# Performance work log

Measured on AMD Instinct MI355X. Metric: run time of the kernel, lower is better.

Reference implementation:

```python
import jax, jax.numpy as jnp
import numpy as np

B, L, DIM, H = 2, 2048, 2048, 16
D = DIM // H  # head_dim = 128
EPS = 1e-6


def _rope_freqs(seq_len: int, head_dim: int, theta: float = 10000.0) -> jnp.ndarray:
    # Flux-style rotation matrix: [1, 1, L, D/2, 2, 2]
    pos = np.arange(seq_len, dtype=np.float32)
    inv = 1.0 / (theta ** (np.arange(0, head_dim, 2, dtype=np.float32) / head_dim))
    ang = np.einsum('l,d->ld', pos, inv)  # [L, D/2]
    cos, sin = np.cos(ang), np.sin(ang)
    rot = np.stack([np.stack([cos, -sin], -1), np.stack([sin, cos], -1)], -2)  # [L, D/2, 2, 2]
    return jnp.asarray(rot[None, None])


def _rms_norm(x, scale):
    rrms = jax.lax.rsqrt(jnp.mean(jnp.square(x), axis=-1, keepdims=True) + EPS)
    return x * rrms * scale


def _apply_rope(xq, xk, freqs_cis):
    # xq/xk: [B, H, L, D]; freqs_cis: [1, 1, L, D/2, 2, 2]
    def rot(x):
        xr = x.reshape(*x.shape[:-1], -1, 1, 2)  # [B,H,L,D/2,1,2]
        out = freqs_cis[..., 0] * xr[..., 0] + freqs_cis[..., 1] * xr[..., 1]
        return out.reshape(x.shape)
    return rot(xq), rot(xk)


def setup_inputs() -> dict:
    key = jax.random.key(0)
    ks = jax.random.split(key, 4)
    x = jax.random.normal(ks[0], (B, L, DIM), dtype=jnp.float32)
    qkv_w = jax.random.normal(ks[1], (DIM, 3 * DIM), dtype=jnp.float32) * 0.02
    qkv_b = jnp.zeros((3 * DIM,), dtype=jnp.float32)
    q_scale = jnp.ones((D,), dtype=jnp.float32)
    k_scale = jnp.ones((D,), dtype=jnp.float32)
    proj_w = jax.random.normal(ks[2], (DIM, DIM), dtype=jnp.float32) * 0.02
    proj_b = jnp.zeros((DIM,), dtype=jnp.float32)
    pe = _rope_freqs(L, D)
    return {"x": x, "pe": pe, "qkv_w": qkv_w, "qkv_b": qkv_b,
            "q_scale": q_scale, "k_scale": k_scale,
            "proj_w": proj_w, "proj_b": proj_b}


def reference(x, pe, qkv_w, qkv_b, q_scale, k_scale, proj_w, proj_b):
    b, l, _ = x.shape
    qkv = x @ qkv_w + qkv_b                      # [B, L, 3*DIM]
    qkv = qkv.reshape(b, l, 3, H, D)
    qkv = jnp.transpose(qkv, (2, 0, 3, 1, 4))    # [3, B, H, L, D]
    q, k, v = qkv[0], qkv[1], qkv[2]
    q = _rms_norm(q, q_scale)
    k = _rms_norm(k, k_scale)
    q, k = _apply_rope(q, k, pe)
    scores = jnp.einsum('bhqd,bhkd->bhqk', q, k) / jnp.sqrt(jnp.float32(D))
    attn = jax.nn.softmax(scores, axis=-1)
    o = jnp.einsum('bhqk,bhkd->bhqd', attn, v)   # [B, H, L, D]
    o = jnp.transpose(o, (0, 2, 1, 3)).reshape(b, l, H * D)
    return o @ proj_w + proj_b
```

## Files before the change

kernel.cpp:

```cpp
#include <hip/hip_runtime.h>
#include <cstdint>
#include <cstddef>

#define BB 2
#define HB 16
#define LL 2048
#define DD 128
#define MM 4096
#define KK 2048
#define N1 6144
#define N2 2048
#define BHLD (BB*HB*LL*DD)

typedef unsigned short u16;
typedef __bf16 bf16x8 __attribute__((ext_vector_type(8)));
typedef short  s16x4  __attribute__((ext_vector_type(4)));
typedef float  f32x4  __attribute__((ext_vector_type(4)));

typedef __attribute__((address_space(1))) void* as1_ptr;
typedef __attribute__((address_space(3))) void* as3_ptr;

__device__ __forceinline__ void gload16(const void* g, void* l) {
  __builtin_amdgcn_global_load_lds((as1_ptr)g, (as3_ptr)l, 16, 0, 0);
}

__device__ __forceinline__ float bf2f(u16 u) {
  union { unsigned v; float f; } c; c.v = ((unsigned)u) << 16; return c.f;
}
__device__ __forceinline__ u16 f2bf(float f) {
  unsigned u = __builtin_bit_cast(unsigned, f);
  return (u16)((u + 0x7FFFu + ((u >> 16) & 1u)) >> 16);
}


__global__ __launch_bounds__(256) void f32_to_bf16_vec(
    const float* __restrict__ in, u16* __restrict__ out, int n4) {
  int i = blockIdx.x * 256 + threadIdx.x;
  if (i >= n4) return;
  float4 v = ((const float4*)in)[i];
  ushort4 o;
  o.x = f2bf(v.x); o.y = f2bf(v.y); o.z = f2bf(v.z); o.w = f2bf(v.w);
  ((ushort4*)out)[i] = o;
}

__global__ __launch_bounds__(256) void transpose_f32_bf16(
    const float* __restrict__ in, u16* __restrict__ out, int R, int C) {
  __shared__ float t[32][33];
  int c0 = blockIdx.x * 32, r0 = blockIdx.y * 32;
  int tx = threadIdx.x & 31, ty = threadIdx.x >> 5;
#pragma unroll
  for (int i = ty; i < 32; i += 8)
    t[i][tx] = in[(size_t)(r0 + i) * C + c0 + tx];
  __syncthreads();
#pragma unroll
  for (int i = ty; i < 32; i += 8)
    out[(size_t)(c0 + i) * R + r0 + tx] = f2bf(t[tx][i]);
}

template<int MODE>
__global__ __launch_bounds__(256) void gemm_bt(
    const u16* __restrict__ A, const u16* __restrict__ Bt,
    const float* __restrict__ bias, void* __restrict__ Cout,
    int Msz, int Nsz, int Ksz)
{
  __shared__ __align__(16) u16 As[128*64];
  __shared__ __align__(16) u16 Bs[128*64];
  const int tid  = threadIdx.x;
  const int lane = tid & 63;
  const int wid  = tid >> 6;
  const int l15  = lane & 15, quad = lane >> 4;
  const int m0 = blockIdx.y * 128, n0 = blockIdx.x * 128;
  const int wm = (wid >> 1) * 64, wn = (wid & 1) * 64;

  f32x4 acc[4][4] = {};

  for (int ks = 0; ks < Ksz; ks += 64) {
    __syncthreads();
#pragma unroll
    for (int j = 0; j < 4; j++) {
      const int s = (wid*4 + j)*64 + lane;
      const int row = s >> 3, pc = (s & 7) ^ (row & 7);
      gload16(&A [(size_t)(m0 + row) * Ksz + ks + pc*8], &As[(wid*4 + j)*512]);
      gload16(&Bt[(size_t)(n0 + row) * Ksz + ks + pc*8], &Bs[(wid*4 + j)*512]);
    }
    __syncthreads();
#pragma unroll
    for (int kh = 0; kh < 2; kh++) {
      bf16x8 af[4], bfr[4];
#pragma unroll
      for (int i = 0; i < 4; i++) {
        const int r = wm + i*16 + l15;
        af[i]  = *(const bf16x8*)&As[r*64 + (((kh*4 + quad) ^ (r & 7)))*8];
      }
#pragma unroll
      for (int i = 0; i < 4; i++) {
        const int r = wn + i*16 + l15;
        bfr[i] = *(const bf16x8*)&Bs[r*64 + (((kh*4 + quad) ^ (r & 7)))*8];
      }
#pragma unroll
      for (int i = 0; i < 4; i++)
#pragma unroll
        for (int j = 0; j < 4; j++)
          acc[i][j] = __builtin_amdgcn_mfma_f32_16x16x32_bf16(af[i], bfr[j], acc[i][j], 0, 0, 0);
    }
  }

#pragma unroll
  for (int i = 0; i < 4; i++) {
#pragma unroll
    for (int j = 0; j < 4; j++) {
      const int col = n0 + wn + j*16 + l15;
      const float bv = bias[col];
#pragma unroll
      for (int r = 0; r < 4; r++) {
        const int row = m0 + wm + i*16 + quad*4 + r;
        float v = acc[i][j][r] + bv;
        if (MODE == 0) {
          u16* qkv = (u16*)Cout;
          int t = col >> 11, hd = col & 2047, h = hd >> 7, d = hd & 127;
          int b = row >> 11, l = row & (LL - 1);
          size_t dst;
          if (t < 2) dst = (size_t)t * BHLD + (((size_t)(b*HB + h)) * LL + l) * DD + d;
          else       dst = (size_t)2 * BHLD + (((size_t)(b*HB + h)) * DD + d) * LL + l;
          qkv[dst] = f2bf(v);
        } else {
          ((float*)Cout)[(size_t)row * Nsz + col] = v;
        }
      }
    }
  }
}

__global__ __launch_bounds__(256) void norm_rope(
    u16* __restrict__ qkv, const float* __restrict__ pe,
    const float* __restrict__ qsc, const float* __restrict__ ksc)
{
  const int wid = threadIdx.x >> 6, lane = threadIdx.x & 63;
  const int r = blockIdx.x * 4 + wid;
  const int l = r & (LL - 1);
  const float4 p4 = *(const float4*)&pe[((size_t)l * 64 + lane) * 4];
#pragma unroll
  for (int t = 0; t < 2; t++) {
    u16* base = qkv + (size_t)t * BHLD + (size_t)r * DD + lane * 2;
    const float* sc = t ? ksc : qsc;
    ushort2 xx = *(const ushort2*)base;
    float x0 = bf2f(xx.x), x1 = bf2f(xx.y);
    float ss = x0*x0 + x1*x1;
#pragma unroll
    for (int m = 1; m < 64; m <<= 1) ss += __shfl_xor(ss, m, 64);
    float rr = rsqrtf(ss * (1.0f/128.0f) + 1e-6f);
    if (t == 0) rr *= 0.08838834764831845f;
    float y0 = x0 * rr * sc[lane*2], y1 = x1 * rr * sc[lane*2 + 1];
    ushort2 oo;
    oo.x = f2bf(p4.x * y0 + p4.y * y1);
    oo.y = f2bf(p4.z * y0 + p4.w * y1);
    *(ushort2*)base = oo;
  }
}

#define BKT 64
__global__ __launch_bounds__(256, 2) void attn(
    const u16* __restrict__ qkv, u16* __restrict__ Oout)
{
  __shared__ __align__(16) u16 Ksh[2][BKT * DD];
  __shared__ __align__(16) u16 Vsh[2][DD * BKT];

  const int bh = blockIdx.x & 31, qt = blockIdx.x >> 5;
  const int wid = threadIdx.x >> 6, lane = threadIdx.x & 63;
  const int l15 = lane & 15, quad = lane >> 4;
  const int q0 = qt * 128 + wid * 32;
  const u16* qp = qkv + (size_t)bh * LL * DD;
  const u16* kp = qkv + (size_t)BHLD + (size_t)bh * LL * DD;
  const u16* vp = qkv + (size_t)2 * BHLD + (size_t)bh * DD * LL;

  bf16x8 qb[2][4];
#pragma unroll
  for (int qf = 0; qf < 2; qf++)
#pragma unroll
    for (int f = 0; f < 4; f++)
      qb[qf][f] = *(const bf16x8*)&qp[(size_t)(q0 + qf*16 + l15) * DD + f*32 + quad*8];

  float l_acc[2] = {0.f, 0.f};
  f32x4 oacc[2][8] = {};

  auto stage = [&](int buf, int k0) {
#pragma unroll
    for (int j = 0; j < 4; j++) {
      const int s = (wid*4 + j)*64 + lane;
      {
        const int r = s >> 4, c = s & 15;
        const int lc = (c & 8) | ((c & 7) ^ (r & 7));
        gload16(&kp[(size_t)(k0 + r) * DD + lc*8], &Ksh[buf][(wid*4 + j)*512]);
      }
      {
        const int r = s >> 3, c = s & 7;
        const int lc = c ^ (r & 7);
        gload16(&vp[(size_t)r * LL + k0 + lc*8], &Vsh[buf][(wid*4 + j)*512]);
      }
    }
  };

  stage(0, 0);
  int cur = 0;

  for (int k0 = 0; k0 < LL; k0 += BKT) {
    __syncthreads();

    f32x4 s[2][4] = {};
#pragma unroll
    for (int f = 0; f < 4; f++) {
      bf16x8 kf[4];
#pragma unroll
      for (int mt = 0; mt < 4; mt++) {
        const int rr = mt*16 + l15;
        const int Lc = f*4 + quad;
        const int pc = (Lc & 8) | ((Lc & 7) ^ (rr & 7));
        kf[mt] = *(const bf16x8*)&Ksh[cur][rr*DD + pc*8];
      }
#pragma unroll
      for (int qf = 0; qf < 2; qf++)
#pragma unroll
        for (int mt = 0; mt < 4; mt++)
          s[qf][mt] = __builtin_amdgcn_mfma_f32_16x16x32_bf16(kf[mt], qb[qf][f], s[qf][mt], 0, 0, 0);
    }

    s16x4 vb[4][8];
#pragma unroll
    for (int t = 0; t < 4; t++)
#pragma unroll
      for (int c = 0; c < 8; c++) {
        const int rv = c*16 + l15;
        const int pc = (t*2 + (quad >> 1)) ^ (l15 & 7);
        vb[t][c] = *(const s16x4*)&Vsh[cur][rv*BKT + pc*8 + (quad & 1)*4];
      }

    if (k0 + BKT < LL) stage(cur ^ 1, k0 + BKT);

    s16x4 pa[2][4];
#pragma unroll
    for (int qf = 0; qf < 2; qf++) {
#pragma unroll
      for (int mt = 0; mt < 4; mt++) {
        float p0 = __expf(s[qf][mt][0] - 12.f);
        float p1 = __expf(s[qf][mt][1] - 12.f);
        float p2 = __expf(s[qf][mt][2] - 12.f);
        float p3 = __expf(s[qf][mt][3] - 12.f);
        l_acc[qf] += (p0 + p1) + (p2 + p3);
        pa[qf][mt][0] = (short)f2bf(p0); pa[qf][mt][1] = (short)f2bf(p1);
        pa[qf][mt][2] = (short)f2bf(p2); pa[qf][mt][3] = (short)f2bf(p3);
      }
    }

#pragma unroll
    for (int t = 0; t < 4; t++)
#pragma unroll
      for (int qf = 0; qf < 2; qf++)
#pragma unroll
        for (int c = 0; c < 8; c++)
          oacc[qf][c] = __builtin_amdgcn_mfma_f32_16x16x16bf16_1k(pa[qf][t], vb[t][c], oacc[qf][c], 0, 0, 0);

    cur ^= 1;
  }

#pragma unroll
  for (int qf = 0; qf < 2; qf++) {
    l_acc[qf] += __shfl_xor(l_acc[qf], 16, 64);
    l_acc[qf] += __shfl_xor(l_acc[qf], 32, 64);
  }
  const int b = bh >> 4, h = bh & 15;
#pragma unroll
  for (int qf = 0; qf < 2; qf++) {
    float lr[4];
#pragma unroll
    for (int r = 0; r < 4; r++)
      lr[r] = 1.0f / __shfl(l_acc[qf], (quad << 4) | (quad*4 + r), 64);
#pragma unroll
    for (int c = 0; c < 8; c++)
#pragma unroll
      for (int r = 0; r < 4; r++) {
        int qrow = q0 + qf*16 + quad*4 + r;
        Oout[((size_t)(b*LL + qrow)) * N2 + h*DD + c*16 + l15] = f2bf(oacc[qf][c][r] * lr[r]);
      }
  }
}


extern "C" void kernel_launch(void* const* d_in, const int* in_sizes, int n_in,
                              void* d_out, int out_size, void* d_ws, size_t ws_size,
                              hipStream_t stream) {
  const float* x       = (const float*)d_in[0];
  const float* pe      = (const float*)d_in[1];
  const float* qkv_w   = (const float*)d_in[2];
  const float* qkv_b   = (const float*)d_in[3];
  const float* q_scale = (const float*)d_in[4];
  const float* k_scale = (const float*)d_in[5];
  const float* proj_w  = (const float*)d_in[6];
  const float* proj_b  = (const float*)d_in[7];

  char* ws = (char*)d_ws;
  u16* xb   = (u16*)(ws + 0);
  u16* w1t  = (u16*)(ws + 16777216);
  u16* w2t  = (u16*)(ws + 41943040);
  u16* qkv  = (u16*)(ws + 50331648);
  u16* attO = (u16*)(ws + 100663296);

  f32_to_bf16_vec<<<(MM*KK/4)/256, 256, 0, stream>>>(x, xb, MM*KK/4);
  transpose_f32_bf16<<<dim3(N1/32, KK/32), 256, 0, stream>>>(qkv_w, w1t, KK, N1);
  transpose_f32_bf16<<<dim3(N2/32, KK/32), 256, 0, stream>>>(proj_w, w2t, KK, N2);
  gemm_bt<0><<<dim3(N1/128, MM/128), 256, 0, stream>>>(xb, w1t, qkv_b, (void*)qkv, MM, N1, KK);
  norm_rope<<<(BB*HB*LL)/4, 256, 0, stream>>>(qkv, pe, q_scale, k_scale);
  attn<<<BB*HB*(LL/128), 256, 0, stream>>>(qkv, attO);
  gemm_bt<1><<<dim3(N2/128, MM/128), 256, 0, stream>>>(attO, w2t, proj_b, d_out, MM, N2, KK);
}
```

Baseline: 442.0 us.

## Fuse RMSNorm+RoPE into QKV GEMM epilogue and merge prep kernels

Folds the per-head RMS norm and rotary embedding into the QKV GEMM epilogue. The row sum of squares is reduced across lanes and across the two N-halves of each 128-column block through shared memory, so the separate norm_rope pass that re-read and re-wrote Q and K is removed. The three conversion/transpose kernels are also merged into one launch to cut launch overhead. In exchange the epilogue gains extra shuffles, two block barriers, and per-element pe loads.

```diff
diff --git a/kernel.cpp b/kernel.cpp
--- a/kernel.cpp
+++ b/kernel.cpp
@@ -32,36 +32,42 @@
   return (u16)((u + 0x7FFFu + ((u >> 16) & 1u)) >> 16);
 }
 
-
-__global__ __launch_bounds__(256) void f32_to_bf16_vec(
-    const float* __restrict__ in, u16* __restrict__ out, int n4) {
-  int i = blockIdx.x * 256 + threadIdx.x;
-  if (i >= n4) return;
-  float4 v = ((const float4*)in)[i];
-  ushort4 o;
-  o.x = f2bf(v.x); o.y = f2bf(v.y); o.z = f2bf(v.z); o.w = f2bf(v.w);
-  ((ushort4*)out)[i] = o;
-}
-
-__global__ __launch_bounds__(256) void transpose_f32_bf16(
-    const float* __restrict__ in, u16* __restrict__ out, int R, int C) {
+__global__ __launch_bounds__(256) void prep(
+    const float* __restrict__ x,  u16* __restrict__ xb,
+    const float* __restrict__ w1, u16* __restrict__ w1t,
+    const float* __restrict__ w2, u16* __restrict__ w2t)
+{
   __shared__ float t[32][33];
-  int c0 = blockIdx.x * 32, r0 = blockIdx.y * 32;
-  int tx = threadIdx.x & 31, ty = threadIdx.x >> 5;
+  const int bid = blockIdx.x;
+  if (bid < 8192) {
+    int i = bid * 256 + threadIdx.x;
+    float4 v = ((const float4*)x)[i];
+    ushort4 o;
+    o.x = f2bf(v.x); o.y = f2bf(v.y); o.z = f2bf(v.z); o.w = f2bf(v.w);
+    ((ushort4*)xb)[i] = o;
+    return;
+  }
+  const float* in; u16* out; int C, idx;
+  if (bid < 20480) { idx = bid - 8192;  in = w1; out = w1t; C = N1; }
+  else             { idx = bid - 20480; in = w2; out = w2t; C = N2; }
+  const int xt = C / 32;
+  const int c0 = (idx % xt) * 32, r0 = (idx / xt) * 32;
+  const int tx = threadIdx.x & 31, ty = threadIdx.x >> 5;
 #pragma unroll
   for (int i = ty; i < 32; i += 8)
     t[i][tx] = in[(size_t)(r0 + i) * C + c0 + tx];
   __syncthreads();
 #pragma unroll
   for (int i = ty; i < 32; i += 8)
-    out[(size_t)(c0 + i) * R + r0 + tx] = f2bf(t[tx][i]);
+    out[(size_t)(c0 + i) * KK + r0 + tx] = f2bf(t[tx][i]);
 }
 
 template<int MODE>
 __global__ __launch_bounds__(256) void gemm_bt(
     const u16* __restrict__ A, const u16* __restrict__ Bt,
     const float* __restrict__ bias, void* __restrict__ Cout,
-    int Msz, int Nsz, int Ksz)
+    const float* __restrict__ pe, const float* __restrict__ qsc,
+    const float* __restrict__ ksc, int Msz, int Nsz, int Ksz)
 {
   __shared__ __align__(16) u16 As[128*64];
   __shared__ __align__(16) u16 Bs[128*64];
@@ -105,57 +111,97 @@
     }
   }
 
-#pragma unroll
-  for (int i = 0; i < 4; i++) {
+  if (MODE == 1) {
+#pragma unroll
+    for (int i = 0; i < 4; i++)
+#pragma unroll
+      for (int j = 0; j < 4; j++) {
+        const int col = n0 + wn + j*16 + l15;
+        const float bv = bias[col];
+#pragma unroll
+        for (int r = 0; r < 4; r++) {
+          const int row = m0 + wm + i*16 + quad*4 + r;
+          ((float*)Cout)[(size_t)row * Nsz + col] = acc[i][j][r] + bv;
+        }
+      }
+    return;
+  }
+
+  u16* qkv = (u16*)Cout;
+  const int t = n0 >> 11;
+  const int h = (n0 >> 7) & 15;
+  float bv[4];
+#pragma unroll
+  for (int j = 0; j < 4; j++) bv[j] = bias[n0 + wn + j*16 + l15];
+
+  if (t == 2) {
+#pragma unroll
+    for (int i = 0; i < 4; i++)
+#pragma unroll
+      for (int j = 0; j < 4; j++) {
+        const int d = wn + j*16 + l15;
+#pragma unroll
+        for (int r = 0; r < 4; r++) {
+          const int row = m0 + wm + i*16 + quad*4 + r;
+          const int b = row >> 11, l = row & (LL - 1);
+          qkv[(size_t)2*BHLD + (((size_t)(b*HB + h))*DD + d)*LL + l] = f2bf(acc[i][j][r] + bv[j]);
+        }
+      }
+    return;
+  }
+
+  float ss[4][4];
+#pragma unroll
+  for (int i = 0; i < 4; i++)
+#pragma unroll
+    for (int r = 0; r < 4; r++) {
+      float s = 0.f;
+#pragma unroll
+      for (int j = 0; j < 4; j++) { float v = acc[i][j][r] + bv[j]; s += v*v; }
+      s += __shfl_xor(s, 1, 64); s += __shfl_xor(s, 2, 64);
+      s += __shfl_xor(s, 4, 64); s += __shfl_xor(s, 8, 64);
+      ss[i][r] = s;
+    }
+  __syncthreads();
+  float* sp = (float*)As;
+  if (l15 == 0) {
+#pragma unroll
+    for (int i = 0; i < 4; i++)
+#pragma unroll
+      for (int r = 0; r < 4; r++) sp[wid*64 + i*16 + quad*4 + r] = ss[i][r];
+  }
+  __syncthreads();
+  float rrms[4][4];
+  const float qfac = 0.08838834764831845f;
+#pragma unroll
+  for (int i = 0; i < 4; i++)
+#pragma unroll
+    for (int r = 0; r < 4; r++) {
+      const float tot = ss[i][r] + sp[(wid^1)*64 + i*16 + quad*4 + r];
+      float rr = rsqrtf(tot * (1.0f/128.0f) + 1e-6f);
+      if (t == 0) rr *= qfac;
+      rrms[i][r] = rr;
+    }
+  const float* scp = t ? ksc : qsc;
+  float scv[4];
+#pragma unroll
+  for (int j = 0; j < 4; j++) scv[j] = scp[wn + j*16 + l15];
+#pragma unroll
+  for (int i = 0; i < 4; i++)
 #pragma unroll
     for (int j = 0; j < 4; j++) {
-      const int col = n0 + wn + j*16 + l15;
-      const float bv = bias[col];
+      const int d = wn + j*16 + l15;
 #pragma unroll
       for (int r = 0; r < 4; r++) {
         const int row = m0 + wm + i*16 + quad*4 + r;
-        float v = acc[i][j][r] + bv;
-        if (MODE == 0) {
-          u16* qkv = (u16*)Cout;
-          int t = col >> 11, hd = col & 2047, h = hd >> 7, d = hd & 127;
-          int b = row >> 11, l = row & (LL - 1);
-          size_t dst;
-          if (t < 2) dst = (size_t)t * BHLD + (((size_t)(b*HB + h)) * LL + l) * DD + d;
-          else       dst = (size_t)2 * BHLD + (((size_t)(b*HB + h)) * DD + d) * LL + l;
-          qkv[dst] = f2bf(v);
-        } else {
-          ((float*)Cout)[(size_t)row * Nsz + col] = v;
-        }
-      }
-    }
-  }
-}
-
-__global__ __launch_bounds__(256) void norm_rope(
-    u16* __restrict__ qkv, const float* __restrict__ pe,
-    const float* __restrict__ qsc, const float* __restrict__ ksc)
-{
-  const int wid = threadIdx.x >> 6, lane = threadIdx.x & 63;
-  const int r = blockIdx.x * 4 + wid;
-  const int l = r & (LL - 1);
-  const float4 p4 = *(const float4*)&pe[((size_t)l * 64 + lane) * 4];
-#pragma unroll
-  for (int t = 0; t < 2; t++) {
-    u16* base = qkv + (size_t)t * BHLD + (size_t)r * DD + lane * 2;
-    const float* sc = t ? ksc : qsc;
-    ushort2 xx = *(const ushort2*)base;
-    float x0 = bf2f(xx.x), x1 = bf2f(xx.y);
-    float ss = x0*x0 + x1*x1;
-#pragma unroll
-    for (int m = 1; m < 64; m <<= 1) ss += __shfl_xor(ss, m, 64);
-    float rr = rsqrtf(ss * (1.0f/128.0f) + 1e-6f);
-    if (t == 0) rr *= 0.08838834764831845f;
-    float y0 = x0 * rr * sc[lane*2], y1 = x1 * rr * sc[lane*2 + 1];
-    ushort2 oo;
-    oo.x = f2bf(p4.x * y0 + p4.y * y1);
-    oo.y = f2bf(p4.z * y0 + p4.w * y1);
-    *(ushort2*)base = oo;
-  }
+        const int b = row >> 11, l = row & (LL - 1);
+        const float y  = (acc[i][j][r] + bv[j]) * rrms[i][r] * scv[j];
+        const float yo = __shfl_xor(y, 1, 64);
+        const float4 p4 = *(const float4*)&pe[((size_t)l*64 + (d >> 1)) * 4];
+        const float o = (l15 & 1) ? (p4.w*y + p4.z*yo) : (p4.x*y + p4.y*yo);
+        qkv[(size_t)t*BHLD + (((size_t)(b*HB + h))*LL + l)*DD + d] = f2bf(o);
+      }
+    }
 }
 
 #define BKT 64
@@ -226,19 +272,19 @@
 
     s16x4 vb[4][8];
 #pragma unroll
-    for (int t = 0; t < 4; t++)
+    for (int tt = 0; tt < 4; tt++)
 #pragma unroll
       for (int c = 0; c < 8; c++) {
         const int rv = c*16 + l15;
-        const int pc = (t*2 + (quad >> 1)) ^ (l15 & 7);
-        vb[t][c] = *(const s16x4*)&Vsh[cur][rv*BKT + pc*8 + (quad & 1)*4];
+        const int pc = (tt*2 + (quad >> 1)) ^ (l15 & 7);
+        vb[tt][c] = *(const s16x4*)&Vsh[cur][rv*BKT + pc*8 + (quad & 1)*4];
       }
 
     if (k0 + BKT < LL) stage(cur ^ 1, k0 + BKT);
 
     s16x4 pa[2][4];
 #pragma unroll
-    for (int qf = 0; qf < 2; qf++) {
+    for (int qf = 0; qf < 2; qf++)
 #pragma unroll
       for (int mt = 0; mt < 4; mt++) {
         float p0 = __expf(s[qf][mt][0] - 12.f);
@@ -249,15 +295,14 @@
         pa[qf][mt][0] = (short)f2bf(p0); pa[qf][mt][1] = (short)f2bf(p1);
         pa[qf][mt][2] = (short)f2bf(p2); pa[qf][mt][3] = (short)f2bf(p3);
       }
-    }
-
-#pragma unroll
-    for (int t = 0; t < 4; t++)
+
+#pragma unroll
+    for (int tt = 0; tt < 4; tt++)
 #pragma unroll
       for (int qf = 0; qf < 2; qf++)
 #pragma unroll
         for (int c = 0; c < 8; c++)
-          oacc[qf][c] = __builtin_amdgcn_mfma_f32_16x16x16bf16_1k(pa[qf][t], vb[t][c], oacc[qf][c], 0, 0, 0);
+          oacc[qf][c] = __builtin_amdgcn_mfma_f32_16x16x16bf16_1k(pa[qf][tt], vb[tt][c], oacc[qf][c], 0, 0, 0);
 
     cur ^= 1;
   }
@@ -304,11 +349,10 @@
   u16* qkv  = (u16*)(ws + 50331648);
   u16* attO = (u16*)(ws + 100663296);
 
-  f32_to_bf16_vec<<<(MM*KK/4)/256, 256, 0, stream>>>(x, xb, MM*KK/4);
-  transpose_f32_bf16<<<dim3(N1/32, KK/32), 256, 0, stream>>>(qkv_w, w1t, KK, N1);
-  transpose_f32_bf16<<<dim3(N2/32, KK/32), 256, 0, stream>>>(proj_w, w2t, KK, N2);
-  gemm_bt<0><<<dim3(N1/128, MM/128), 256, 0, stream>>>(xb, w1t, qkv_b, (void*)qkv, MM, N1, KK);
-  norm_rope<<<(BB*HB*LL)/4, 256, 0, stream>>>(qkv, pe, q_scale, k_scale);
+  prep<<<24576, 256, 0, stream>>>(x, xb, qkv_w, w1t, proj_w, w2t);
+  gemm_bt<0><<<dim3(N1/128, MM/128), 256, 0, stream>>>(
+      xb, w1t, qkv_b, (void*)qkv, pe, q_scale, k_scale, MM, N1, KK);
   attn<<<BB*HB*(LL/128), 256, 0, stream>>>(qkv, attO);
-  gemm_bt<1><<<dim3(N2/128, MM/128), 256, 0, stream>>>(attO, w2t, proj_b, d_out, MM, N2, KK);
-}
+  gemm_bt<1><<<dim3(N2/128, MM/128), 256, 0, stream>>>(
+      attO, w2t, proj_b, d_out, nullptr, nullptr, nullptr, MM, N2, KK);
+}
```

Measured after the change: 637.6 us. +44.3%, slower.
